# Kernel tuning notes

Hardware: AMD Instinct MI355X
Metric: run time of the kernel (lower is better)

## Reference

```python
import jax, jax.numpy as jnp
import numpy as np


def setup_inputs() -> dict:
    key = jax.random.key(0)
    k1, k2, k3, k4 = jax.random.split(key, 4)
    B, L1, L2, H, A = 64, 512, 512, 1024, 1024
    reps_lt = jax.random.normal(k1, (B, L1, H), dtype=jnp.float32)
    reps_rt = jax.random.normal(k2, (B, L2, H), dtype=jnp.float32)
    mask_lt = jnp.ones((B, L1), dtype=jnp.float32)
    mask_rt = jnp.ones((B, L2), dtype=jnp.float32)
    # Keras 'uniform' initializer ~ U(-0.05, 0.05); scale similarly
    attn_w1 = jax.random.uniform(k3, (H, A), dtype=jnp.float32, minval=-0.05, maxval=0.05)
    diagonal_W = jax.random.uniform(k4, (1, 1, A), dtype=jnp.float32, minval=-0.05, maxval=0.05)
    return {
        "reps_lt": reps_lt,
        "reps_rt": reps_rt,
        "mask_lt": mask_lt,
        "mask_rt": mask_rt,
        "attn_w1": attn_w1,
        "diagonal_W": diagonal_W,
    }


def reference(reps_lt, reps_rt, mask_lt, mask_rt, attn_w1, diagonal_W):
    # Projections: the original does expand_dims + broadcast multiply + sum,
    # which is mathematically a matmul over the hidden dim.
    # attn_w2 aliases attn_w1 because hidden dims are equal.
    attn_lt = jnp.tanh(jnp.einsum('blh,ha->bla', reps_lt, attn_w1))  # [B,L1,A]
    attn_rt = jnp.tanh(jnp.einsum('brh,ha->bra', reps_rt, attn_w1))  # [B,L2,A]
    attn_lt = attn_lt * diagonal_W                                   # diagonal bilinear scale
    # batch_dot([B,L1,A], [B,A,L2]) -> [B,L1,L2]
    attn_value = jnp.einsum('bla,bra->blr', attn_lt, attn_rt)
    # mask (multiplicative, as in original) before softmax
    attn_value = attn_value * mask_lt[:, :, None] * mask_rt[:, None, :]
    attn_prob = jax.nn.softmax(attn_value, axis=-1)
    # mask again after softmax
    attn_prob = attn_prob * mask_lt[:, :, None] * mask_rt[:, None, :]
    return attn_prob
```

## Files before the change

kernel.cpp:

```cpp
#include <hip/hip_runtime.h>
#include <hip/hip_bf16.h>

#define B_ 64
#define L_ 512
#define H_ 1024
#define A_ 1024

typedef short bf16x8 __attribute__((ext_vector_type(8)));
typedef float f32x4 __attribute__((ext_vector_type(4)));

__device__ __forceinline__ void gld16(const void* g, void* l) {
  __builtin_amdgcn_global_load_lds((const __attribute__((address_space(1))) void*)g,
                                   (__attribute__((address_space(3))) void*)l, 16, 0, 0);
}

__device__ __forceinline__ unsigned short f2bf(float f) {
  unsigned u = __builtin_bit_cast(unsigned, f);
  u = (u + 0x7fffu + ((u >> 16) & 1u)) >> 16;
  return (unsigned short)u;
}

__device__ __forceinline__ unsigned short cvtbf(float f) {
  __hip_bfloat16 b = __float2bfloat16(f);
  return __builtin_bit_cast(unsigned short, b);
}

__device__ __forceinline__ float fast_tanh(float x) {
  float e = __expf(2.f * x);
  float r = __builtin_amdgcn_rcpf(e + 1.f);
  return __builtin_fmaf(-2.f, r, 1.f);
}

__global__ __launch_bounds__(256) void cvt_kernel(const float* __restrict__ lt,
                                                  const float* __restrict__ rt,
                                                  unsigned short* __restrict__ xb) {
  const size_t NC = (size_t)B_ * L_ * H_ / 8;
  size_t stride = (size_t)gridDim.x * blockDim.x;
  for (size_t c = (size_t)blockIdx.x * blockDim.x + threadIdx.x; c < 2 * NC; c += stride) {
    const float* src = (c < NC) ? (lt + c * 8) : (rt + (c - NC) * 8);
    float4 v0 = ((const float4*)src)[0];
    float4 v1 = ((const float4*)src)[1];
    bf16x8 o;
    o[0] = (short)cvtbf(v0.x); o[1] = (short)cvtbf(v0.y);
    o[2] = (short)cvtbf(v0.z); o[3] = (short)cvtbf(v0.w);
    o[4] = (short)cvtbf(v1.x); o[5] = (short)cvtbf(v1.y);
    o[6] = (short)cvtbf(v1.z); o[7] = (short)cvtbf(v1.w);
    *(bf16x8*)(xb + c * 8) = o;
  }
}

__global__ __launch_bounds__(256) void wtrans_kernel(const float* __restrict__ W,
                                                     unsigned short* __restrict__ Wt) {
  __shared__ float tile[32][33];
  int tx = threadIdx.x & 31, ty = threadIdx.x >> 5;
  int a0 = (blockIdx.x & 31) << 5, h0 = (blockIdx.x >> 5) << 5;
#pragma unroll
  for (int i = 0; i < 4; ++i) {
    int h = ty + i * 8;
    tile[h][tx] = W[(size_t)(h0 + h) * A_ + a0 + tx];
  }
  __syncthreads();
#pragma unroll
  for (int i = 0; i < 4; ++i) {
    int a = ty + i * 8;
    Wt[(size_t)(a0 + a) * H_ + h0 + tx] = f2bf(tile[tx][a]);
  }
}

__global__ __launch_bounds__(512, 2) void proj8_kernel(
    const unsigned short* __restrict__ Xb, const unsigned short* __restrict__ Wt,
    const float* __restrict__ diag, unsigned short* __restrict__ Pb) {
  __shared__ unsigned short As[2][256 * 64];
  __shared__ unsigned short Bs[2][256 * 64];
  int t = threadIdx.x;
  int lane = t & 63, wave = t >> 6;
  int wr = wave >> 2, wcn = wave & 3;
  int l15 = lane & 15, l4 = lane >> 4;

  int bid = (int)blockIdx.x;
  int x = bid & 7, k = bid >> 3;
  int mt = x + 8 * (k >> 2);
  int nt = k & 3;
  int mrow0 = mt << 8;
  int ncol0 = nt << 8;
  int isLt = (mt < 128);

  int r0 = t >> 3;
  int swzc = (((t & 7) ^ (r0 & 7)) << 3);
  const unsigned short* A0 = Xb + (size_t)(mrow0 + r0) * H_ + swzc;
  const unsigned short* B0 = Wt + (size_t)(ncol0 + r0) * H_ + swzc;

#define STAGE(buf, koff)                                                   \
  {                                                                        \
    _Pragma("unroll") for (int i = 0; i < 4; ++i) {                        \
      gld16(A0 + (size_t)i * 64 * H_ + (koff), &As[buf][(i * 512 + t) * 8]); \
      gld16(B0 + (size_t)i * 64 * H_ + (koff), &Bs[buf][(i * 512 + t) * 8]); \
    }                                                                      \
  }

  f32x4 acc[8][4] = {};
  int rdsw0 = ((0 * 4 + l4) ^ (l15 & 7)) * 8;
  int rdsw1 = ((1 * 4 + l4) ^ (l15 & 7)) * 8;

  STAGE(0, 0);
  int cur = 0;
  for (int kt = 0; kt < 16; ++kt) {
    if (kt < 15) {
      STAGE(cur ^ 1, (kt + 1) * 64);
      asm volatile("s_waitcnt vmcnt(8)" ::: "memory");
    } else {
      asm volatile("s_waitcnt vmcnt(0)" ::: "memory");
    }
    asm volatile("s_barrier" ::: "memory");

    const unsigned short* Ac = As[cur];
    const unsigned short* Bc = Bs[cur];
    bf16x8 bq[4][2];
#pragma unroll
    for (int ni = 0; ni < 4; ++ni) {
      int brow = wcn * 64 + ni * 16 + l15;
      bq[ni][0] = *(const bf16x8*)&Bc[brow * 64 + rdsw0];
      bq[ni][1] = *(const bf16x8*)&Bc[brow * 64 + rdsw1];
    }
#pragma unroll
    for (int ph = 0; ph < 4; ++ph) {
      bf16x8 aq[2][2];
#pragma unroll
      for (int m2 = 0; m2 < 2; ++m2) {
        int arow = wr * 128 + (ph * 2 + m2) * 16 + l15;
        aq[m2][0] = *(const bf16x8*)&Ac[arow * 64 + rdsw0];
        aq[m2][1] = *(const bf16x8*)&Ac[arow * 64 + rdsw1];
      }
      __builtin_amdgcn_s_setprio(1);
#pragma unroll
      for (int m2 = 0; m2 < 2; ++m2)
#pragma unroll
        for (int ni = 0; ni < 4; ++ni) {
          acc[ph * 2 + m2][ni] = __builtin_amdgcn_mfma_f32_16x16x32_bf16(
              aq[m2][0], bq[ni][0], acc[ph * 2 + m2][ni], 0, 0, 0);
          acc[ph * 2 + m2][ni] = __builtin_amdgcn_mfma_f32_16x16x32_bf16(
              aq[m2][1], bq[ni][1], acc[ph * 2 + m2][ni], 0, 0, 0);
        }
      __builtin_amdgcn_s_setprio(0);
    }
    asm volatile("s_barrier" ::: "memory");
    cur ^= 1;
  }
#undef STAGE

#pragma unroll
  for (int mi = 0; mi < 8; ++mi) {
#pragma unroll
    for (int ni = 0; ni < 4; ++ni) {
      int col = ncol0 + wcn * 64 + ni * 16 + l15;
      float d = isLt ? diag[col] : 1.0f;
#pragma unroll
      for (int rr = 0; rr < 4; ++rr) {
        int row = mrow0 + wr * 128 + mi * 16 + l4 * 4 + rr;
        Pb[(size_t)row * A_ + col] = f2bf(fast_tanh(acc[mi][ni][rr]) * d);
      }
    }
  }
}

__global__ __launch_bounds__(256) void score_kernel(
    const unsigned short* __restrict__ Plt, const unsigned short* __restrict__ Prt,
    const float* __restrict__ mask_lt, const float* __restrict__ mask_rt,
    float* __restrict__ out) {
  __shared__ unsigned short As[128 * 64];
  __shared__ unsigned short Bs[128 * 64];
  int t = threadIdx.x;
  int lane = t & 63, wave = t >> 6;
  int wr = wave >> 1, wc = wave & 1;
  int l15 = lane & 15, l4 = lane >> 4;

  int bid = (int)blockIdx.x;
  int x = bid & 7, k = bid >> 3;
  int atile = x + 8 * (k >> 2);
  int b = atile >> 2, tm = atile & 3, tn = k & 3;

  const unsigned short* Abase = Plt + (size_t)b * L_ * A_ + (size_t)(tm * 128) * A_;
  const unsigned short* Bbase = Prt + (size_t)b * L_ * A_ + (size_t)(tn * 128) * A_;

  const unsigned short* asrc[4];
  const unsigned short* bsrc[4];
  int dst[4];
#pragma unroll
  for (int i = 0; i < 4; ++i) {
    int c = i * 256 + t;
    int r = c >> 3, kc = c & 7;
    int sc = (kc ^ (r & 7)) * 8;
    asrc[i] = &Abase[(size_t)r * A_ + sc];
    bsrc[i] = &Bbase[(size_t)r * A_ + sc];
    dst[i] = c * 8;
  }
  int swz0 = ((0 * 4 + l4) ^ (l15 & 7)) * 8;
  int swz1 = ((1 * 4 + l4) ^ (l15 & 7)) * 8;

  f32x4 acc[4][4] = {};
  for (int kt = 0; kt < A_ / 64; ++kt) {
    int k0 = kt * 64;
    __syncthreads();
#pragma unroll
    for (int i = 0; i < 4; ++i) {
      gld16(asrc[i] + k0, &As[dst[i]]);
      gld16(bsrc[i] + k0, &Bs[dst[i]]);
    }
    __syncthreads();
#pragma unroll
    for (int kk = 0; kk < 2; ++kk) {
      int sw = kk ? swz1 : swz0;
      bf16x8 aq[4], bq[4];
#pragma unroll
      for (int mi = 0; mi < 4; ++mi)
        aq[mi] = *(const bf16x8*)&As[(wr * 64 + mi * 16 + l15) * 64 + sw];
#pragma unroll
      for (int ni = 0; ni < 4; ++ni)
        bq[ni] = *(const bf16x8*)&Bs[(wc * 64 + ni * 16 + l15) * 64 + sw];
#pragma unroll
      for (int mi = 0; mi < 4; ++mi)
#pragma unroll
        for (int ni = 0; ni < 4; ++ni)
          acc[mi][ni] = __builtin_amdgcn_mfma_f32_16x16x32_bf16(aq[mi], bq[ni], acc[mi][ni], 0, 0, 0);
    }
  }
  const float* mlp = mask_lt + b * L_;
  const float* mrp = mask_rt + b * L_;
  float* obase = out + (size_t)b * L_ * L_;
#pragma unroll
  for (int mi = 0; mi < 4; ++mi) {
#pragma unroll
    for (int ni = 0; ni < 4; ++ni) {
      int col = tn * 128 + wc * 64 + ni * 16 + l15;
      float mr = mrp[col];
#pragma unroll
      for (int r = 0; r < 4; ++r) {
        int row = tm * 128 + wr * 64 + mi * 16 + l4 * 4 + r;
        obase[(size_t)row * L_ + col] = acc[mi][ni][r] * mlp[row] * mr;
      }
    }
  }
}

__global__ __launch_bounds__(256) void softmax_kernel(float* __restrict__ out,
                                                      const float* __restrict__ mask_lt,
                                                      const float* __restrict__ mask_rt) {
  int lane = threadIdx.x & 63, wave = threadIdx.x >> 6;
  int row = (int)blockIdx.x * 4 + wave;
  int b = row >> 9;
  float* p = out + (size_t)row * L_;
  float4 v0 = *(const float4*)(p + lane * 8);
  float4 v1 = *(const float4*)(p + lane * 8 + 4);
  float m = fmaxf(fmaxf(fmaxf(v0.x, v0.y), fmaxf(v0.z, v0.w)),
                  fmaxf(fmaxf(v1.x, v1.y), fmaxf(v1.z, v1.w)));
#pragma unroll
  for (int off = 32; off; off >>= 1) m = fmaxf(m, __shfl_xor(m, off));
  float e0 = __expf(v0.x - m), e1 = __expf(v0.y - m), e2 = __expf(v0.z - m), e3 = __expf(v0.w - m);
  float e4 = __expf(v1.x - m), e5 = __expf(v1.y - m), e6 = __expf(v1.z - m), e7 = __expf(v1.w - m);
  float s = ((e0 + e1) + (e2 + e3)) + ((e4 + e5) + (e6 + e7));
#pragma unroll
  for (int off = 32; off; off >>= 1) s += __shfl_xor(s, off);
  float sc = (1.0f / s) * mask_lt[row];
  const float* mrp = mask_rt + (b << 9) + lane * 8;
  float4 mr0 = *(const float4*)mrp;
  float4 mr1 = *(const float4*)(mrp + 4);
  float4 o0 = make_float4(e0 * sc * mr0.x, e1 * sc * mr0.y, e2 * sc * mr0.z, e3 * sc * mr0.w);
  float4 o1 = make_float4(e4 * sc * mr1.x, e5 * sc * mr1.y, e6 * sc * mr1.z, e7 * sc * mr1.w);
  *(float4*)(p + lane * 8) = o0;
  *(float4*)(p + lane * 8 + 4) = o1;
}

extern "C" void kernel_launch(void* const* d_in, const int* in_sizes, int n_in,
                              void* d_out, int out_size, void* d_ws, size_t ws_size,
                              hipStream_t stream) {
  const float* reps_lt = (const float*)d_in[0];
  const float* reps_rt = (const float*)d_in[1];
  const float* mask_lt = (const float*)d_in[2];
  const float* mask_rt = (const float*)d_in[3];
  const float* attn_w1 = (const float*)d_in[4];
  const float* diag    = (const float*)d_in[5];
  float* out = (float*)d_out;

  unsigned short* wt  = (unsigned short*)d_ws;
  unsigned short* pb  = wt + (size_t)H_ * A_;
  unsigned short* xb  = pb + (size_t)B_ * L_ * A_ * 2;
  unsigned short* plt = pb;
  unsigned short* prt = pb + (size_t)B_ * L_ * A_;

  hipLaunchKernelGGL(wtrans_kernel, dim3(1024), dim3(256), 0, stream, attn_w1, wt);
  hipLaunchKernelGGL(cvt_kernel, dim3(8192), dim3(256), 0, stream,
                     reps_lt, reps_rt, xb);
  hipLaunchKernelGGL(proj8_kernel, dim3(1024), dim3(512), 0, stream,
                     xb, wt, diag, pb);
  hipLaunchKernelGGL(score_kernel, dim3(1024), dim3(256), 0, stream,
                     plt, prt, mask_lt, mask_rt, out);
  hipLaunchKernelGGL(softmax_kernel, dim3(8192), dim3(256), 0, stream,
                     out, mask_lt, mask_rt);
}
```

Baseline: 341.3 us.

## Fuse fp32-to-bf16 input conversion into projection GEMM A-tile loading

```diff
diff --git a/kernel.cpp b/kernel.cpp
--- a/kernel.cpp
+++ b/kernel.cpp
@@ -29,24 +29,6 @@
   float e = __expf(2.f * x);
   float r = __builtin_amdgcn_rcpf(e + 1.f);
   return __builtin_fmaf(-2.f, r, 1.f);
-}
-
-__global__ __launch_bounds__(256) void cvt_kernel(const float* __restrict__ lt,
-                                                  const float* __restrict__ rt,
-                                                  unsigned short* __restrict__ xb) {
-  const size_t NC = (size_t)B_ * L_ * H_ / 8;
-  size_t stride = (size_t)gridDim.x * blockDim.x;
-  for (size_t c = (size_t)blockIdx.x * blockDim.x + threadIdx.x; c < 2 * NC; c += stride) {
-    const float* src = (c < NC) ? (lt + c * 8) : (rt + (c - NC) * 8);
-    float4 v0 = ((const float4*)src)[0];
-    float4 v1 = ((const float4*)src)[1];
-    bf16x8 o;
-    o[0] = (short)cvtbf(v0.x); o[1] = (short)cvtbf(v0.y);
-    o[2] = (short)cvtbf(v0.z); o[3] = (short)cvtbf(v0.w);
-    o[4] = (short)cvtbf(v1.x); o[5] = (short)cvtbf(v1.y);
-    o[6] = (short)cvtbf(v1.z); o[7] = (short)cvtbf(v1.w);
-    *(bf16x8*)(xb + c * 8) = o;
-  }
 }
 
 __global__ __launch_bounds__(256) void wtrans_kernel(const float* __restrict__ W,
@@ -68,8 +50,9 @@
 }
 
 __global__ __launch_bounds__(512, 2) void proj8_kernel(
-    const unsigned short* __restrict__ Xb, const unsigned short* __restrict__ Wt,
-    const float* __restrict__ diag, unsigned short* __restrict__ Pb) {
+    const float* __restrict__ Xlt, const float* __restrict__ Xrt,
+    const unsigned short* __restrict__ Wt, const float* __restrict__ diag,
+    unsigned short* __restrict__ Pb) {
   __shared__ unsigned short As[2][256 * 64];
   __shared__ unsigned short Bs[2][256 * 64];
   int t = threadIdx.x;
@@ -84,34 +67,58 @@
   int mrow0 = mt << 8;
   int ncol0 = nt << 8;
   int isLt = (mt < 128);
+  const float* X = isLt ? Xlt : Xrt;
+  int xrow0 = (isLt ? mt : mt - 128) << 8;
+
+  int ra = t >> 1, kh = t & 1;
+  const float* Asrc = X + (size_t)(xrow0 + ra) * H_ + kh * 32;
+  int awoff[4];
+#pragma unroll
+  for (int c = 0; c < 4; ++c)
+    awoff[c] = (ra * 8 + ((kh * 4 + c) ^ (ra & 7))) * 8;
 
   int r0 = t >> 3;
-  int swzc = (((t & 7) ^ (r0 & 7)) << 3);
-  const unsigned short* A0 = Xb + (size_t)(mrow0 + r0) * H_ + swzc;
+  int swzc = ((t & 7) ^ (r0 & 7)) << 3;
   const unsigned short* B0 = Wt + (size_t)(ncol0 + r0) * H_ + swzc;
 
-#define STAGE(buf, koff)                                                   \
+  f32x4 acc[8][4] = {};
+  int rdsw0 = (l4 ^ (l15 & 7)) * 8;
+  int rdsw1 = ((4 + l4) ^ (l15 & 7)) * 8;
+
+  float4 a0[8];
+
+#define CVT_WRITE(buf)                                                     \
   {                                                                        \
-    _Pragma("unroll") for (int i = 0; i < 4; ++i) {                        \
-      gld16(A0 + (size_t)i * 64 * H_ + (koff), &As[buf][(i * 512 + t) * 8]); \
-      gld16(B0 + (size_t)i * 64 * H_ + (koff), &Bs[buf][(i * 512 + t) * 8]); \
+    _Pragma("unroll") for (int c = 0; c < 4; ++c) {                        \
+      bf16x8 v;                                                            \
+      v[0] = (short)cvtbf(a0[2 * c].x); v[1] = (short)cvtbf(a0[2 * c].y);  \
+      v[2] = (short)cvtbf(a0[2 * c].z); v[3] = (short)cvtbf(a0[2 * c].w);  \
+      v[4] = (short)cvtbf(a0[2 * c + 1].x); v[5] = (short)cvtbf(a0[2 * c + 1].y); \
+      v[6] = (short)cvtbf(a0[2 * c + 1].z); v[7] = (short)cvtbf(a0[2 * c + 1].w); \
+      *(bf16x8*)&As[buf][awoff[c]] = v;                                    \
     }                                                                      \
   }
 
-  f32x4 acc[8][4] = {};
-  int rdsw0 = ((0 * 4 + l4) ^ (l15 & 7)) * 8;
-  int rdsw1 = ((1 * 4 + l4) ^ (l15 & 7)) * 8;
-
-  STAGE(0, 0);
+#pragma unroll
+  for (int j = 0; j < 8; ++j) a0[j] = ((const float4*)Asrc)[j];
+#pragma unroll
+  for (int i = 0; i < 4; ++i)
+    gld16(B0 + (size_t)i * 64 * H_, &Bs[0][(i * 512 + t) * 8]);
+  CVT_WRITE(0);
+  asm volatile("s_waitcnt vmcnt(0) lgkmcnt(0)" ::: "memory");
+  asm volatile("s_barrier" ::: "memory");
+
   int cur = 0;
   for (int kt = 0; kt < 16; ++kt) {
-    if (kt < 15) {
-      STAGE(cur ^ 1, (kt + 1) * 64);
-      asm volatile("s_waitcnt vmcnt(8)" ::: "memory");
-    } else {
-      asm volatile("s_waitcnt vmcnt(0)" ::: "memory");
-    }
-    asm volatile("s_barrier" ::: "memory");
+    bool more = (kt < 15);
+    int nk = (kt + 1) * 64;
+    if (more) {
+#pragma unroll
+      for (int j = 0; j < 8; ++j) a0[j] = ((const float4*)(Asrc + nk))[j];
+#pragma unroll
+      for (int i = 0; i < 4; ++i)
+        gld16(B0 + (size_t)i * 64 * H_ + nk, &Bs[cur ^ 1][(i * 512 + t) * 8]);
+    }
 
     const unsigned short* Ac = As[cur];
     const unsigned short* Bc = Bs[cur];
@@ -143,10 +150,13 @@
         }
       __builtin_amdgcn_s_setprio(0);
     }
+
+    if (more) CVT_WRITE(cur ^ 1);
+    asm volatile("s_waitcnt vmcnt(0) lgkmcnt(0)" ::: "memory");
     asm volatile("s_barrier" ::: "memory");
     cur ^= 1;
   }
-#undef STAGE
+#undef CVT_WRITE
 
 #pragma unroll
   for (int mi = 0; mi < 8; ++mi) {
@@ -283,15 +293,12 @@
 
   unsigned short* wt  = (unsigned short*)d_ws;
   unsigned short* pb  = wt + (size_t)H_ * A_;
-  unsigned short* xb  = pb + (size_t)B_ * L_ * A_ * 2;
   unsigned short* plt = pb;
   unsigned short* prt = pb + (size_t)B_ * L_ * A_;
 
   hipLaunchKernelGGL(wtrans_kernel, dim3(1024), dim3(256), 0, stream, attn_w1, wt);
-  hipLaunchKernelGGL(cvt_kernel, dim3(8192), dim3(256), 0, stream,
-                     reps_lt, reps_rt, xb);
   hipLaunchKernelGGL(proj8_kernel, dim3(1024), dim3(512), 0, stream,
-                     xb, wt, diag, pb);
+                     reps_lt, reps_rt, wt, diag, pb);
   hipLaunchKernelGGL(score_kernel, dim3(1024), dim3(256), 0, stream,
                      plt, prt, mask_lt, mask_rt, out);
   hipLaunchKernelGGL(softmax_kernel, dim3(8192), dim3(256), 0, stream,
```

After: 379.6 us. 11.2% more time.

## Use 4-stage K=32 LDS ring with single barrier in projection GEMM

Applied to the files above, without the earlier changes.

```diff
diff --git a/kernel.cpp b/kernel.cpp
--- a/kernel.cpp
+++ b/kernel.cpp
@@ -70,8 +70,8 @@
 __global__ __launch_bounds__(512, 2) void proj8_kernel(
     const unsigned short* __restrict__ Xb, const unsigned short* __restrict__ Wt,
     const float* __restrict__ diag, unsigned short* __restrict__ Pb) {
-  __shared__ unsigned short As[2][256 * 64];
-  __shared__ unsigned short Bs[2][256 * 64];
+  __shared__ unsigned short As4[4][256 * 32];
+  __shared__ unsigned short Bs4[4][256 * 32];
   int t = threadIdx.x;
   int lane = t & 63, wave = t >> 6;
   int wr = wave >> 2, wcn = wave & 3;
@@ -85,68 +85,65 @@
   int ncol0 = nt << 8;
   int isLt = (mt < 128);
 
-  int r0 = t >> 3;
-  int swzc = (((t & 7) ^ (r0 & 7)) << 3);
-  const unsigned short* A0 = Xb + (size_t)(mrow0 + r0) * H_ + swzc;
-  const unsigned short* B0 = Wt + (size_t)(ncol0 + r0) * H_ + swzc;
-
-#define STAGE(buf, koff)                                                   \
-  {                                                                        \
-    _Pragma("unroll") for (int i = 0; i < 4; ++i) {                        \
-      gld16(A0 + (size_t)i * 64 * H_ + (koff), &As[buf][(i * 512 + t) * 8]); \
-      gld16(B0 + (size_t)i * 64 * H_ + (koff), &Bs[buf][(i * 512 + t) * 8]); \
-    }                                                                      \
+  const unsigned short* asrc[2];
+  const unsigned short* bsrc[2];
+#pragma unroll
+  for (int i = 0; i < 2; ++i) {
+    int ci = i * 512 + t;
+    int r = ci >> 2, c = ci & 3;
+    int sc = (c ^ ((r & 3) ^ ((r >> 2) & 3))) << 3;
+    asrc[i] = Xb + (size_t)(mrow0 + r) * H_ + sc;
+    bsrc[i] = Wt + (size_t)(ncol0 + r) * H_ + sc;
+  }
+
+#define STAGE4(buf, kt_)                                        \
+  {                                                             \
+    int ko = (kt_) * 32;                                        \
+    gld16(asrc[0] + ko, &As4[buf][t * 8]);                      \
+    gld16(asrc[1] + ko, &As4[buf][(512 + t) * 8]);              \
+    gld16(bsrc[0] + ko, &Bs4[buf][t * 8]);                      \
+    gld16(bsrc[1] + ko, &Bs4[buf][(512 + t) * 8]);              \
   }
 
   f32x4 acc[8][4] = {};
-  int rdsw0 = ((0 * 4 + l4) ^ (l15 & 7)) * 8;
-  int rdsw1 = ((1 * 4 + l4) ^ (l15 & 7)) * 8;
-
-  STAGE(0, 0);
-  int cur = 0;
-  for (int kt = 0; kt < 16; ++kt) {
-    if (kt < 15) {
-      STAGE(cur ^ 1, (kt + 1) * 64);
+  int rdsw = (l4 ^ ((l15 & 3) ^ ((l15 >> 2) & 3))) * 8;
+
+  STAGE4(0, 0);
+  STAGE4(1, 1);
+  STAGE4(2, 2);
+
+  for (int j = 0; j < 32; ++j) {
+    if (j < 30)
       asm volatile("s_waitcnt vmcnt(8)" ::: "memory");
-    } else {
+    else if (j == 30)
+      asm volatile("s_waitcnt vmcnt(4)" ::: "memory");
+    else
       asm volatile("s_waitcnt vmcnt(0)" ::: "memory");
-    }
     asm volatile("s_barrier" ::: "memory");
-
-    const unsigned short* Ac = As[cur];
-    const unsigned short* Bc = Bs[cur];
-    bf16x8 bq[4][2];
-#pragma unroll
-    for (int ni = 0; ni < 4; ++ni) {
-      int brow = wcn * 64 + ni * 16 + l15;
-      bq[ni][0] = *(const bf16x8*)&Bc[brow * 64 + rdsw0];
-      bq[ni][1] = *(const bf16x8*)&Bc[brow * 64 + rdsw1];
-    }
+    if (j <= 28) STAGE4((j + 3) & 3, j + 3);
+
+    const unsigned short* Ac = As4[j & 3];
+    const unsigned short* Bc = Bs4[j & 3];
+    bf16x8 bq[4];
+#pragma unroll
+    for (int ni = 0; ni < 4; ++ni)
+      bq[ni] = *(const bf16x8*)&Bc[(wcn * 64 + ni * 16 + l15) * 32 + rdsw];
 #pragma unroll
     for (int ph = 0; ph < 4; ++ph) {
-      bf16x8 aq[2][2];
-#pragma unroll
-      for (int m2 = 0; m2 < 2; ++m2) {
-        int arow = wr * 128 + (ph * 2 + m2) * 16 + l15;
-        aq[m2][0] = *(const bf16x8*)&Ac[arow * 64 + rdsw0];
-        aq[m2][1] = *(const bf16x8*)&Ac[arow * 64 + rdsw1];
+      bf16x8 aq0 = *(const bf16x8*)&Ac[(wr * 128 + (ph * 2) * 16 + l15) * 32 + rdsw];
+      bf16x8 aq1 = *(const bf16x8*)&Ac[(wr * 128 + (ph * 2 + 1) * 16 + l15) * 32 + rdsw];
+      __builtin_amdgcn_s_setprio(1);
+#pragma unroll
+      for (int ni = 0; ni < 4; ++ni) {
+        acc[ph * 2][ni] = __builtin_amdgcn_mfma_f32_16x16x32_bf16(
+            aq0, bq[ni], acc[ph * 2][ni], 0, 0, 0);
+        acc[ph * 2 + 1][ni] = __builtin_amdgcn_mfma_f32_16x16x32_bf16(
+            aq1, bq[ni], acc[ph * 2 + 1][ni], 0, 0, 0);
       }
-      __builtin_amdgcn_s_setprio(1);
-#pragma unroll
-      for (int m2 = 0; m2 < 2; ++m2)
-#pragma unroll
-        for (int ni = 0; ni < 4; ++ni) {
-          acc[ph * 2 + m2][ni] = __builtin_amdgcn_mfma_f32_16x16x32_bf16(
-              aq[m2][0], bq[ni][0], acc[ph * 2 + m2][ni], 0, 0, 0);
-          acc[ph * 2 + m2][ni] = __builtin_amdgcn_mfma_f32_16x16x32_bf16(
-              aq[m2][1], bq[ni][1], acc[ph * 2 + m2][ni], 0, 0, 0);
-        }
       __builtin_amdgcn_s_setprio(0);
     }
-    asm volatile("s_barrier" ::: "memory");
-    cur ^= 1;
-  }
-#undef STAGE
+  }
+#undef STAGE4
 
 #pragma unroll
   for (int mi = 0; mi < 8; ++mi) {
```

New measurement: 364.5 us. +6.8%, slower.
